# Optimization experiments

Hardware: AMD Instinct MI355X
Metric: run time of the kernel (lower is better)

Reference implementation:

```python
import jax, jax.numpy as jnp
import numpy as np

N_NODES = 50000
N_EDGES = 800000
IN_DIM = 128
HID = 32
HEADS = 3
OUT_DIM = 128
NEG_SLOPE = 0.2  # PyG GATConv default leaky_relu slope
EPS = 1e-16


def setup_inputs() -> dict:
    key = jax.random.key(0)
    ks = jax.random.split(key, 16)
    x = jax.random.normal(ks[0], (N_NODES, IN_DIM), jnp.float32)
    edge_index = jax.random.randint(ks[1], (2, N_EDGES), 0, N_NODES, dtype=jnp.int32)
    s = 0.1
    return {
        'x': x,
        'edge_index': edge_index,
        # layer 1: in=128 -> heads=3, c=32, concat
        'W1': jax.random.normal(ks[2], (IN_DIM, HEADS * HID), jnp.float32) * s,
        'as1': jax.random.normal(ks[3], (HEADS, HID), jnp.float32) * s,
        'ad1': jax.random.normal(ks[4], (HEADS, HID), jnp.float32) * s,
        'b1': jnp.zeros((HEADS * HID,), jnp.float32),
        # layer 2: in=96 -> heads=3, c=32, concat
        'W2': jax.random.normal(ks[5], (HEADS * HID, HEADS * HID), jnp.float32) * s,
        'as2': jax.random.normal(ks[6], (HEADS, HID), jnp.float32) * s,
        'ad2': jax.random.normal(ks[7], (HEADS, HID), jnp.float32) * s,
        'b2': jnp.zeros((HEADS * HID,), jnp.float32),
        # layer 3: in=96 -> heads=1, c=128, mean (concat=False)
        'W3': jax.random.normal(ks[8], (HEADS * HID, OUT_DIM), jnp.float32) * s,
        'as3': jax.random.normal(ks[9], (1, OUT_DIM), jnp.float32) * s,
        'ad3': jax.random.normal(ks[10], (1, OUT_DIM), jnp.float32) * s,
        'b3': jnp.zeros((OUT_DIM,), jnp.float32),
    }


def _gat_layer(x, src, dst, W, a_s, a_d, b, concat):
    # x: [N, F_in]; src/dst: [E'] (self-loops already appended)
    n = x.shape[0]
    heads, c = a_s.shape
    h = (x @ W).reshape(n, heads, c)                      # [N, H, C]
    alpha_src = jnp.sum(h * a_s[None], axis=-1)           # [N, H]
    alpha_dst = jnp.sum(h * a_d[None], axis=-1)           # [N, H]
    e = jax.nn.leaky_relu(alpha_src[src] + alpha_dst[dst], NEG_SLOPE)  # [E', H]
    # segment softmax over incoming edges of each dst node
    m = jax.ops.segment_max(e, dst, num_segments=n)       # [N, H] (every node has a self-loop)
    e = jnp.exp(e - m[dst])
    denom = jax.ops.segment_sum(e, dst, num_segments=n)   # [N, H]
    alpha = e / (denom[dst] + EPS)                        # [E', H]
    # attention dropout: module is evaluated in inference mode -> identity
    out = jax.ops.segment_sum(alpha[:, :, None] * h[src], dst, num_segments=n)  # [N, H, C]
    out = out.reshape(n, heads * c) if concat else out.mean(axis=1)
    return out + b


def reference(x, edge_index, W1, as1, ad1, b1, W2, as2, ad2, b2, W3, as3, ad3, b3):
    n = x.shape[0]
    loops = jnp.arange(n, dtype=edge_index.dtype)
    src = jnp.concatenate([edge_index[0], loops])  # PyG add_self_loops=True
    dst = jnp.concatenate([edge_index[1], loops])
    h = _gat_layer(x, src, dst, W1, as1, ad1, b1, concat=True)
    h = jax.nn.elu(h)
    h = _gat_layer(h, src, dst, W2, as2, ad2, b2, concat=True)
    h = jax.nn.elu(h)
    out = _gat_layer(h, src, dst, W3, as3, ad3, b3, concat=False)
    return out
```

## Files before the change

### kernel.cpp

```cpp
#include <hip/hip_runtime.h>
#include <hip/hip_bf16.h>
#include <hip/hip_fp16.h>
#include <math.h>

#define N_NODES_C 50000
#define NBKT ((N_NODES_C + 255) / 256)
#define NEG_SLOPE 0.2f
#define EPS_ 1e-16f

typedef _Float16 f16x8 __attribute__((ext_vector_type(8)));
typedef float    f32x4 __attribute__((ext_vector_type(4)));

__device__ __forceinline__ float lrelu(float x){ return x > 0.f ? x : NEG_SLOPE * x; }

__global__ void hist_k(const int* __restrict__ dstv, int* __restrict__ counts, int E){
  int t = blockIdx.x * blockDim.x + threadIdx.x;
  if (t < E) atomicAdd(&counts[dstv[t]], 1);
}

__global__ void chunksum_k(const int* __restrict__ counts, int* __restrict__ sums, int n){
  __shared__ int lds[4];
  int base = blockIdx.x * 1024;
  int t = threadIdx.x;
  int s = 0;
  for (int i = t; i < 1024; i += 256){ int idx = base + i; s += (idx < n) ? counts[idx] : 0; }
  for (int d = 32; d >= 1; d >>= 1) s += __shfl_xor(s, d);
  if ((t & 63) == 0) lds[t >> 6] = s;
  __syncthreads();
  if (t == 0) sums[blockIdx.x] = lds[0] + lds[1] + lds[2] + lds[3];
}

__global__ void scan_k(const int* __restrict__ counts, const int* __restrict__ csums,
                       int* __restrict__ row_ptr, int* __restrict__ bcur, int nch, int n){
  __shared__ int ws[16];
  __shared__ int boff;
  int base = blockIdx.x * 1024; int t = threadIdx.x; int idx = base + t;
  int v = (idx < n) ? counts[idx] : 0;
  int lane = t & 63, wid = t >> 6;
  int x = v;
  for (int d = 1; d < 64; d <<= 1){ int y = __shfl_up(x, d); if (lane >= d) x += y; }
  if (lane == 63) ws[wid] = x;
  if (t < 64){
    int c = (t < blockIdx.x) ? csums[t] : 0;
    for (int d = 32; d >= 1; d >>= 1) c += __shfl_xor(c, d);
    if (t == 0) boff = c;
  }
  __syncthreads();
  if (t < 16){ int y = ws[t]; for (int d = 1; d < 16; d <<= 1){ int z = __shfl_up(y, d); if (t >= d) y += z; } ws[t] = y; }
  __syncthreads();
  int excl = x - v + (wid ? ws[wid - 1] : 0) + boff;
  if (idx < n){
    row_ptr[idx] = excl;
    if ((idx & 255) == 0) bcur[idx >> 8] = excl;
  }
  if (blockIdx.x == nch - 1 && t == 0) row_ptr[n] = boff + ws[15];
}

#define BATCH 2048
#define BCAP 32
__global__ __launch_bounds__(256) void bucket_k(const int* __restrict__ srcv, const int* __restrict__ dstv,
                                                int* __restrict__ bcur, unsigned* __restrict__ ebuf, int E){
  __shared__ unsigned stage[NBKT * BCAP];
  __shared__ int cnt[NBKT];
  int t = threadIdx.x;
  int start = blockIdx.x * BATCH;
  int end = start + BATCH; if (end > E) end = E;
  for (int i = t; i < NBKT; i += 256) cnt[i] = 0;
  __syncthreads();
  for (int e = start + t; e < end; e += 256){
    int s = srcv[e], d = dstv[e];
    int b = d >> 8;
    unsigned entry = (unsigned)s | ((unsigned)(d & 255) << 16);
    int pos = atomicAdd(&cnt[b], 1);
    if (pos < BCAP) stage[b * BCAP + pos] = entry;
    else { int p = atomicAdd(&bcur[b], 1); ebuf[p] = entry; }
  }
  __syncthreads();
  if (t < NBKT){
    int c = cnt[t]; if (c > BCAP) c = BCAP;
    if (c > 0){
      int p = atomicAdd(&bcur[t], c);
      for (int i = 0; i < c; i++) ebuf[p + i] = stage[t * BCAP + i];
    }
  }
}

__global__ __launch_bounds__(256) void bsort_k(const unsigned* __restrict__ ebuf,
                                               const int* __restrict__ row_ptr,
                                               int* __restrict__ esrc, int n){
  __shared__ int cnt[256];
  int b = blockIdx.x;
  int nb = b * 256;
  int t = threadIdx.x;
  cnt[t] = 0;
  __syncthreads();
  int hi_node = nb + 256; if (hi_node > n) hi_node = n;
  int beg = row_ptr[nb], end = row_ptr[hi_node];
  for (int i = beg + t; i < end; i += 256){
    unsigned e = ebuf[i];
    int dl = e >> 16;
    int src = (int)(e & 0xFFFFu);
    int rank = atomicAdd(&cnt[dl], 1);
    esrc[row_ptr[nb + dl] + rank] = src;
  }
}

template<int K, int J>
__device__ void wpack_dev(const float* __restrict__ W, uint4* __restrict__ Wf, int blk, int nblk){
  constexpr int KS = K / 32, NT = J / 16;
  int tot = KS * NT * 64;
  for (int t = blk * 256 + threadIdx.x; t < tot; t += nblk * 256){
    int l = t & 63;
    int nt = (t >> 6) % NT;
    int kk = t / (64 * NT);
    int col = nt * 16 + (l & 15);
    int k0 = kk * 32 + (l >> 4) * 8;
    unsigned u[4];
    #pragma unroll
    for (int p = 0; p < 4; p++){
      __half2 h = __floats2half2_rn(W[(k0 + 2 * p) * J + col], W[(k0 + 2 * p + 1) * J + col]);
      u[p] = *reinterpret_cast<unsigned*>(&h);
    }
    uint4 v; v.x = u[0]; v.y = u[1]; v.z = u[2]; v.w = u[3];
    Wf[t] = v;
  }
}

__global__ void wpack_all_k(const float* W1, const float* W2, const float* W3,
                            uint4* Wf1, uint4* Wf2, uint4* Wf3){
  int b = blockIdx.x;
  if (b < 6) wpack_dev<128, 96>(W1, Wf1, b, 6);
  else if (b < 11) wpack_dev<96, 96>(W2, Wf2, b - 6, 5);
  else wpack_dev<96, 128>(W3, Wf3, b - 11, 6);
}

template<int K, int J, int HEADS, bool AF16>
__global__ __launch_bounds__(256) void gemm_mfma_k(
    const void* __restrict__ Ain, const uint4* __restrict__ Wf,
    const float* __restrict__ a_s, const float* __restrict__ a_d,
    __half* __restrict__ Hh, float* __restrict__ asrc, float* __restrict__ adst, int n){
  constexpr int KS = K / 32;
  constexpr int NT = J / 16;
  constexpr int CPR = K / 8;
  constexpr int NTPH = NT / HEADS;
  __shared__ uint4 Alds[64 * 16];
  int t = threadIdx.x;
  int rbase = blockIdx.x * 64;

  for (int i = t; i < 64 * CPR; i += 256){
    int r = i / CPR, c = i % CPR;
    int gr = rbase + r;
    uint4 v = make_uint4(0u, 0u, 0u, 0u);
    if (gr < n){
      if (AF16){
        v = ((const uint4*)Ain)[(size_t)gr * CPR + c];
      } else {
        const float4* af = (const float4*)Ain + (size_t)gr * (K / 4) + c * 2;
        float4 lo = af[0], hi = af[1];
        __half2 p0 = __floats2half2_rn(lo.x, lo.y);
        __half2 p1 = __floats2half2_rn(lo.z, lo.w);
        __half2 p2 = __floats2half2_rn(hi.x, hi.y);
        __half2 p3 = __floats2half2_rn(hi.z, hi.w);
        v.x = *reinterpret_cast<unsigned*>(&p0);
        v.y = *reinterpret_cast<unsigned*>(&p1);
        v.z = *reinterpret_cast<unsigned*>(&p2);
        v.w = *reinterpret_cast<unsigned*>(&p3);
      }
    }
    Alds[r * 16 + (c ^ (r & 7))] = v;
  }
  __syncthreads();

  int l = t & 63;
  int wrow = (t >> 6) * 16;
  int sub = l & 15;
  int lk = l >> 4;
  f32x4 acc[NT];
  #pragma unroll
  for (int i = 0; i < NT; i++) acc[i] = (f32x4){0.f, 0.f, 0.f, 0.f};

  for (int kk = 0; kk < KS; kk++){
    int trow = wrow + sub;
    int c = kk * 4 + lk;
    f16x8 a = *reinterpret_cast<const f16x8*>(&Alds[trow * 16 + (c ^ (trow & 7))]);
    const uint4* wb = Wf + (size_t)(kk * NT) * 64 + l;
    #pragma unroll
    for (int nt = 0; nt < NT; nt++){
      uint4 wv = wb[nt * 64];
      f16x8 bfr = *reinterpret_cast<const f16x8*>(&wv);
      acc[nt] = __builtin_amdgcn_mfma_f32_16x16x32_f16(a, bfr, acc[nt], 0, 0, 0);
    }
  }

  float ps[HEADS][4], pd[HEADS][4];
  #pragma unroll
  for (int h = 0; h < HEADS; h++)
    #pragma unroll
    for (int r = 0; r < 4; r++){ ps[h][r] = 0.f; pd[h][r] = 0.f; }
  #pragma unroll
  for (int nt = 0; nt < NT; nt++){
    int h = nt / NTPH;
    float sa = a_s[nt * 16 + sub];
    float sd = a_d[nt * 16 + sub];
    #pragma unroll
    for (int r = 0; r < 4; r++){ ps[h][r] += acc[nt][r] * sa; pd[h][r] += acc[nt][r] * sd; }
  }
  #pragma unroll
  for (int h = 0; h < HEADS; h++)
    #pragma unroll
    for (int r = 0; r < 4; r++)
      #pragma unroll
      for (int d = 1; d < 16; d <<= 1){
        ps[h][r] += __shfl_xor(ps[h][r], d);
        pd[h][r] += __shfl_xor(pd[h][r], d);
      }

  #pragma unroll
  for (int r = 0; r < 4; r++){
    int gr = rbase + wrow + lk * 4 + r;
    if (gr < n){
      #pragma unroll
      for (int nt = 0; nt < NT; nt++)
        Hh[(size_t)gr * J + nt * 16 + sub] = __float2half(acc[nt][r]);
    }
  }
  #pragma unroll
  for (int h = 0; h < HEADS; h++){
    if (sub == h){
      #pragma unroll
      for (int r = 0; r < 4; r++){
        int gr = rbase + wrow + lk * 4 + r;
        if (gr < n){
          asrc[gr * HEADS + h] = ps[h][r];
          adst[gr * HEADS + h] = pd[h][r];
        }
      }
    }
  }
}

template<int HEADS, int C, bool ELU, bool OUT16>
__global__ void agg_k(const __half* __restrict__ Hh,
                      const float* __restrict__ asrc, const float* __restrict__ adst,
                      const int* __restrict__ row_ptr, const int* __restrict__ esrc,
                      const float* __restrict__ bias, void* __restrict__ outv, int n){
  constexpr int J = HEADS * C;
  constexpr int NL = J / 2;
  constexpr int WL0 = 64 - 8 * HEADS;
  int node = blockIdx.x * (blockDim.x >> 6) + (threadIdx.x >> 6);
  if (node >= n) return;
  int lane = threadIdx.x & 63;
  bool colact = (NL == 64) || (lane < NL);
  int cl = colact ? lane : 0;
  int c0 = 2 * cl;
  int hh = c0 / C;
  const __half2* hp = (const __half2*)Hh;

  int wl = lane - WL0; if (wl < 0) wl = 0;
  int wu, wh;
  if (HEADS == 3){ wu = wl / 3; wh = wl - wu * 3; } else { wu = wl; wh = 0; }

  float ad_own = adst[node * HEADS + hh];
  float ad_w = (HEADS == 3) ? __shfl(ad_own, wh * 16) : ad_own;

  float wself = __expf(lrelu(asrc[node * HEADS + hh] + ad_own));
  float2 hs = __half22float2(hp[(size_t)node * NL + cl]);
  float acc0 = wself * hs.x, acc1 = wself * hs.y, den = wself;

  int beg = row_ptr[node], end = row_ptr[node + 1];
  int e = beg;
  for (; e + 8 <= end; e += 8){
    int s0 = esrc[e],     s1 = esrc[e + 1], s2 = esrc[e + 2], s3 = esrc[e + 3];
    int s4 = esrc[e + 4], s5 = esrc[e + 5], s6 = esrc[e + 6], s7 = esrc[e + 7];
    int ssel = wu < 4 ? (wu < 2 ? (wu == 0 ? s0 : s1) : (wu == 2 ? s2 : s3))
                      : (wu < 6 ? (wu == 4 ? s4 : s5) : (wu == 6 ? s6 : s7));
    float wv = __expf(lrelu(asrc[ssel * HEADS + wh] + ad_w));
    float w0 = __shfl(wv, WL0 + 0 * HEADS + hh);
    float w1 = __shfl(wv, WL0 + 1 * HEADS + hh);
    float w2 = __shfl(wv, WL0 + 2 * HEADS + hh);
    float w3 = __shfl(wv, WL0 + 3 * HEADS + hh);
    float w4 = __shfl(wv, WL0 + 4 * HEADS + hh);
    float w5 = __shfl(wv, WL0 + 5 * HEADS + hh);
    float w6 = __shfl(wv, WL0 + 6 * HEADS + hh);
    float w7 = __shfl(wv, WL0 + 7 * HEADS + hh);
    __half2 u0 = hp[(size_t)s0 * NL + cl];
    __half2 u1 = hp[(size_t)s1 * NL + cl];
    __half2 u2 = hp[(size_t)s2 * NL + cl];
    __half2 u3 = hp[(size_t)s3 * NL + cl];
    __half2 u4 = hp[(size_t)s4 * NL + cl];
    __half2 u5 = hp[(size_t)s5 * NL + cl];
    __half2 u6 = hp[(size_t)s6 * NL + cl];
    __half2 u7 = hp[(size_t)s7 * NL + cl];
    float2 f0 = __half22float2(u0), f1 = __half22float2(u1);
    float2 f2 = __half22float2(u2), f3 = __half22float2(u3);
    float2 f4 = __half22float2(u4), f5 = __half22float2(u5);
    float2 f6 = __half22float2(u6), f7 = __half22float2(u7);
    acc0 += w0 * f0.x; acc1 += w0 * f0.y; den += w0;
    acc0 += w1 * f1.x; acc1 += w1 * f1.y; den += w1;
    acc0 += w2 * f2.x; acc1 += w2 * f2.y; den += w2;
    acc0 += w3 * f3.x; acc1 += w3 * f3.y; den += w3;
    acc0 += w4 * f4.x; acc1 += w4 * f4.y; den += w4;
    acc0 += w5 * f5.x; acc1 += w5 * f5.y; den += w5;
    acc0 += w6 * f6.x; acc1 += w6 * f6.y; den += w6;
    acc0 += w7 * f7.x; acc1 += w7 * f7.y; den += w7;
  }
  for (; e < end; e++){
    int s = esrc[e];
    float w = __expf(lrelu(asrc[s * HEADS + hh] + ad_own));
    float2 h = __half22float2(hp[(size_t)s * NL + cl]);
    acc0 += w * h.x; acc1 += w * h.y; den += w;
  }
  if (colact){
    float inv = 1.f / (den + EPS_);
    float r0 = acc0 * inv + bias[c0];
    float r1 = acc1 * inv + bias[c0 + 1];
    if (ELU){
      r0 = r0 > 0.f ? r0 : __expf(r0) - 1.f;
      r1 = r1 > 0.f ? r1 : __expf(r1) - 1.f;
    }
    if (OUT16){
      ((__half2*)outv)[(size_t)node * NL + cl] = __floats2half2_rn(r0, r1);
    } else {
      *reinterpret_cast<float2*>((float*)outv + (size_t)node * J + c0) = make_float2(r0, r1);
    }
  }
}

extern "C" void kernel_launch(void* const* d_in, const int* in_sizes, int n_in,
                              void* d_out, int out_size, void* d_ws, size_t ws_size,
                              hipStream_t stream){
  const float* x   = (const float*)d_in[0];
  const int*   ei  = (const int*)  d_in[1];
  const float* W1  = (const float*)d_in[2];
  const float* as1 = (const float*)d_in[3];
  const float* ad1 = (const float*)d_in[4];
  const float* b1  = (const float*)d_in[5];
  const float* W2  = (const float*)d_in[6];
  const float* as2 = (const float*)d_in[7];
  const float* ad2 = (const float*)d_in[8];
  const float* b2  = (const float*)d_in[9];
  const float* W3  = (const float*)d_in[10];
  const float* as3 = (const float*)d_in[11];
  const float* ad3 = (const float*)d_in[12];
  const float* b3  = (const float*)d_in[13];
  float* out = (float*)d_out;

  const int N = N_NODES_C;
  const int E = in_sizes[1] / 2;
  const int* srcv = ei;
  const int* dstv = ei + E;

  char* ws = (char*)d_ws;
  auto alloc = [&](size_t bytes)->char*{ char* p = ws; ws += (bytes + 255) & ~(size_t)255; return p; };
  int*      counts  = (int*)     alloc((size_t)N * 4);
  int*      row_ptr = (int*)     alloc((size_t)(N + 1) * 4);
  int*      csums   = (int*)     alloc(64 * 4);
  int*      bcur    = (int*)     alloc(NBKT * 4);
  int*      esrc    = (int*)     alloc((size_t)E * 4);
  unsigned* ebuf    = (unsigned*)alloc((size_t)E * 4);
  __half*   Hh      = (__half*)  alloc((size_t)N * 128 * 2);
  __half*   feat_h  = (__half*)  alloc((size_t)N * 96 * 2);
  float*    a_src   = (float*)   alloc((size_t)N * 3 * 4);
  float*    a_dst   = (float*)   alloc((size_t)N * 3 * 4);
  uint4*    Wf1     = (uint4*)   alloc(128 * 96 * 2);
  uint4*    Wf2     = (uint4*)   alloc(96 * 96 * 2);
  uint4*    Wf3     = (uint4*)   alloc(96 * 128 * 2);

  hipMemsetAsync(counts, 0, (size_t)N * 4, stream);
  hist_k<<<(E + 255) / 256, 256, 0, stream>>>(dstv, counts, E);
  int nch = (N + 1023) / 1024;
  chunksum_k<<<nch, 256, 0, stream>>>(counts, csums, N);
  scan_k<<<nch, 1024, 0, stream>>>(counts, csums, row_ptr, bcur, nch, N);
  bucket_k<<<(E + BATCH - 1) / BATCH, 256, 0, stream>>>(srcv, dstv, bcur, ebuf, E);
  bsort_k<<<NBKT, 256, 0, stream>>>(ebuf, row_ptr, esrc, N);

  wpack_all_k<<<17, 256, 0, stream>>>(W1, W2, W3, Wf1, Wf2, Wf3);

  int gnode4 = (N + 3) / 4;
  int ggemm  = (N + 63) / 64;

  gemm_mfma_k<128, 96, 3, false><<<ggemm, 256, 0, stream>>>(x, Wf1, as1, ad1, Hh, a_src, a_dst, N);
  agg_k<3, 32, true, true><<<gnode4, 256, 0, stream>>>(Hh, a_src, a_dst, row_ptr, esrc, b1, feat_h, N);

  gemm_mfma_k<96, 96, 3, true><<<ggemm, 256, 0, stream>>>(feat_h, Wf2, as2, ad2, Hh, a_src, a_dst, N);
  agg_k<3, 32, true, true><<<gnode4, 256, 0, stream>>>(Hh, a_src, a_dst, row_ptr, esrc, b2, feat_h, N);

  gemm_mfma_k<96, 128, 1, true><<<ggemm, 256, 0, stream>>>(feat_h, Wf3, as3, ad3, Hh, a_src, a_dst, N);
  agg_k<1, 128, false, false><<<gnode4, 256, 0, stream>>>(Hh, a_src, a_dst, row_ptr, esrc, b3, out, N);
}
```

Measured before the change: 326.8 us.

## Aggregate a group of consecutive nodes per wave over a merged edge stream

Self-loops now go into the CSR itself: counts start at 1 and bucket_k emits the loop edges. Each esrc entry keeps the local destination index in its high bits, so every edge's logit is computed from asrc and adst directly. Each wavefront now handles eight consecutive nodes and walks their combined edge range with an 8-wide unrolled loop, writing out each node when its boundary is crossed. The aim is to cut idle lanes and tail loops on low-degree nodes; the cost is the cross-lane weight sharing being dropped, extra per-edge adst loads and a divergent boundary check.

```diff
diff --git a/kernel.cpp b/kernel.cpp
--- a/kernel.cpp
+++ b/kernel.cpp
@@ -12,6 +12,11 @@
 typedef float    f32x4 __attribute__((ext_vector_type(4)));
 
 __device__ __forceinline__ float lrelu(float x){ return x > 0.f ? x : NEG_SLOPE * x; }
+
+__global__ void cinit_k(int* __restrict__ counts, int n){
+  int t = blockIdx.x * blockDim.x + threadIdx.x;
+  if (t < n) counts[t] = 1;
+}
 
 __global__ void hist_k(const int* __restrict__ dstv, int* __restrict__ counts, int E){
   int t = blockIdx.x * blockDim.x + threadIdx.x;
@@ -59,16 +64,20 @@
 #define BATCH 2048
 #define BCAP 32
 __global__ __launch_bounds__(256) void bucket_k(const int* __restrict__ srcv, const int* __restrict__ dstv,
-                                                int* __restrict__ bcur, unsigned* __restrict__ ebuf, int E){
+                                                int* __restrict__ bcur, unsigned* __restrict__ ebuf,
+                                                int E, int n){
   __shared__ unsigned stage[NBKT * BCAP];
   __shared__ int cnt[NBKT];
   int t = threadIdx.x;
+  int tot = E + n;
   int start = blockIdx.x * BATCH;
-  int end = start + BATCH; if (end > E) end = E;
+  int end = start + BATCH; if (end > tot) end = tot;
   for (int i = t; i < NBKT; i += 256) cnt[i] = 0;
   __syncthreads();
-  for (int e = start + t; e < end; e += 256){
-    int s = srcv[e], d = dstv[e];
+  for (int idx = start + t; idx < end; idx += 256){
+    int s, d;
+    if (idx < E){ s = srcv[idx]; d = dstv[idx]; }
+    else { s = idx - E; d = s; }
     int b = d >> 8;
     unsigned entry = (unsigned)s | ((unsigned)(d & 255) << 16);
     int pos = atomicAdd(&cnt[b], 1);
@@ -99,9 +108,8 @@
   for (int i = beg + t; i < end; i += 256){
     unsigned e = ebuf[i];
     int dl = e >> 16;
-    int src = (int)(e & 0xFFFFu);
     int rank = atomicAdd(&cnt[dl], 1);
-    esrc[row_ptr[nb + dl] + rank] = src;
+    esrc[row_ptr[nb + dl] + rank] = (int)e;
   }
 }
 
@@ -239,91 +247,76 @@
   }
 }
 
-template<int HEADS, int C, bool ELU, bool OUT16>
-__global__ void agg_k(const __half* __restrict__ Hh,
-                      const float* __restrict__ asrc, const float* __restrict__ adst,
-                      const int* __restrict__ row_ptr, const int* __restrict__ esrc,
-                      const float* __restrict__ bias, void* __restrict__ outv, int n){
+template<int HEADS, int C, bool ELU, bool OUT16, int GN>
+__global__ __launch_bounds__(256) void agg_k(const __half* __restrict__ Hh,
+    const float* __restrict__ asrc, const float* __restrict__ adst,
+    const int* __restrict__ row_ptr, const int* __restrict__ esrc,
+    const float* __restrict__ bias, void* __restrict__ outv, int n){
   constexpr int J = HEADS * C;
   constexpr int NL = J / 2;
-  constexpr int WL0 = 64 - 8 * HEADS;
-  int node = blockIdx.x * (blockDim.x >> 6) + (threadIdx.x >> 6);
-  if (node >= n) return;
+  int wid = blockIdx.x * (blockDim.x >> 6) + (threadIdx.x >> 6);
+  int n0 = wid * GN;
+  if (n0 >= n) return;
   int lane = threadIdx.x & 63;
-  bool colact = (NL == 64) || (lane < NL);
-  int cl = colact ? lane : 0;
-  int c0 = 2 * cl;
+  if (lane >= NL) return;
+  int c0 = 2 * lane;
   int hh = c0 / C;
   const __half2* hp = (const __half2*)Hh;
-
-  int wl = lane - WL0; if (wl < 0) wl = 0;
-  int wu, wh;
-  if (HEADS == 3){ wu = wl / 3; wh = wl - wu * 3; } else { wu = wl; wh = 0; }
-
-  float ad_own = adst[node * HEADS + hh];
-  float ad_w = (HEADS == 3) ? __shfl(ad_own, wh * 16) : ad_own;
-
-  float wself = __expf(lrelu(asrc[node * HEADS + hh] + ad_own));
-  float2 hs = __half22float2(hp[(size_t)node * NL + cl]);
-  float acc0 = wself * hs.x, acc1 = wself * hs.y, den = wself;
-
-  int beg = row_ptr[node], end = row_ptr[node + 1];
-  int e = beg;
-  for (; e + 8 <= end; e += 8){
-    int s0 = esrc[e],     s1 = esrc[e + 1], s2 = esrc[e + 2], s3 = esrc[e + 3];
-    int s4 = esrc[e + 4], s5 = esrc[e + 5], s6 = esrc[e + 6], s7 = esrc[e + 7];
-    int ssel = wu < 4 ? (wu < 2 ? (wu == 0 ? s0 : s1) : (wu == 2 ? s2 : s3))
-                      : (wu < 6 ? (wu == 4 ? s4 : s5) : (wu == 6 ? s6 : s7));
-    float wv = __expf(lrelu(asrc[ssel * HEADS + wh] + ad_w));
-    float w0 = __shfl(wv, WL0 + 0 * HEADS + hh);
-    float w1 = __shfl(wv, WL0 + 1 * HEADS + hh);
-    float w2 = __shfl(wv, WL0 + 2 * HEADS + hh);
-    float w3 = __shfl(wv, WL0 + 3 * HEADS + hh);
-    float w4 = __shfl(wv, WL0 + 4 * HEADS + hh);
-    float w5 = __shfl(wv, WL0 + 5 * HEADS + hh);
-    float w6 = __shfl(wv, WL0 + 6 * HEADS + hh);
-    float w7 = __shfl(wv, WL0 + 7 * HEADS + hh);
-    __half2 u0 = hp[(size_t)s0 * NL + cl];
-    __half2 u1 = hp[(size_t)s1 * NL + cl];
-    __half2 u2 = hp[(size_t)s2 * NL + cl];
-    __half2 u3 = hp[(size_t)s3 * NL + cl];
-    __half2 u4 = hp[(size_t)s4 * NL + cl];
-    __half2 u5 = hp[(size_t)s5 * NL + cl];
-    __half2 u6 = hp[(size_t)s6 * NL + cl];
-    __half2 u7 = hp[(size_t)s7 * NL + cl];
-    float2 f0 = __half22float2(u0), f1 = __half22float2(u1);
-    float2 f2 = __half22float2(u2), f3 = __half22float2(u3);
-    float2 f4 = __half22float2(u4), f5 = __half22float2(u5);
-    float2 f6 = __half22float2(u6), f7 = __half22float2(u7);
-    acc0 += w0 * f0.x; acc1 += w0 * f0.y; den += w0;
-    acc0 += w1 * f1.x; acc1 += w1 * f1.y; den += w1;
-    acc0 += w2 * f2.x; acc1 += w2 * f2.y; den += w2;
-    acc0 += w3 * f3.x; acc1 += w3 * f3.y; den += w3;
-    acc0 += w4 * f4.x; acc1 += w4 * f4.y; den += w4;
-    acc0 += w5 * f5.x; acc1 += w5 * f5.y; den += w5;
-    acc0 += w6 * f6.x; acc1 += w6 * f6.y; den += w6;
-    acc0 += w7 * f7.x; acc1 += w7 * f7.y; den += w7;
-  }
-  for (; e < end; e++){
-    int s = esrc[e];
-    float w = __expf(lrelu(asrc[s * HEADS + hh] + ad_own));
-    float2 h = __half22float2(hp[(size_t)s * NL + cl]);
-    acc0 += w * h.x; acc1 += w * h.y; den += w;
-  }
-  if (colact){
+  int gcnt = min(GN, n - n0);
+  int rp = row_ptr[n0 + min(lane, gcnt)];
+  float b0 = bias[c0], b1 = bias[c0 + 1];
+  int bkt3 = (n0 & ~255) * HEADS;
+  int e = __shfl(rp, 0);
+  int eend = __shfl(rp, gcnt);
+  int g = 0;
+  int nb = __shfl(rp, 1);
+  float acc0 = 0.f, acc1 = 0.f, den = 0.f;
+  __half2* outh = (__half2*)outv;
+  float* outf = (float*)outv;
+
+  auto finalize = [&](int gg){
     float inv = 1.f / (den + EPS_);
-    float r0 = acc0 * inv + bias[c0];
-    float r1 = acc1 * inv + bias[c0 + 1];
+    float r0 = acc0 * inv + b0, r1 = acc1 * inv + b1;
     if (ELU){
       r0 = r0 > 0.f ? r0 : __expf(r0) - 1.f;
       r1 = r1 > 0.f ? r1 : __expf(r1) - 1.f;
     }
-    if (OUT16){
-      ((__half2*)outv)[(size_t)node * NL + cl] = __floats2half2_rn(r0, r1);
-    } else {
-      *reinterpret_cast<float2*>((float*)outv + (size_t)node * J + c0) = make_float2(r0, r1);
-    }
-  }
+    int node = n0 + gg;
+    if (OUT16) outh[(size_t)node * NL + lane] = __floats2half2_rn(r0, r1);
+    else *reinterpret_cast<float2*>(outf + (size_t)node * J + c0) = make_float2(r0, r1);
+    acc0 = 0.f; acc1 = 0.f; den = 0.f;
+  };
+
+  for (; e + 8 <= eend; e += 8){
+    int ev[8];
+    #pragma unroll
+    for (int u = 0; u < 8; u++) ev[u] = esrc[e + u];
+    float w[8]; float2 f[8];
+    #pragma unroll
+    for (int u = 0; u < 8; u++){
+      int s = ev[u] & 0xFFFF;
+      int dl = ((unsigned)ev[u]) >> 16;
+      float logit = asrc[s * HEADS + hh] + adst[bkt3 + dl * HEADS + hh];
+      w[u] = __expf(lrelu(logit));
+      f[u] = __half22float2(hp[(size_t)s * NL + lane]);
+    }
+    #pragma unroll
+    for (int u = 0; u < 8; u++){
+      while (e + u >= nb && g < gcnt - 1){ finalize(g); g++; nb = __shfl(rp, g + 1); }
+      acc0 += w[u] * f[u].x; acc1 += w[u] * f[u].y; den += w[u];
+    }
+  }
+  for (; e < eend; e++){
+    int ev = esrc[e];
+    int s = ev & 0xFFFF;
+    int dl = ((unsigned)ev) >> 16;
+    while (e >= nb && g < gcnt - 1){ finalize(g); g++; nb = __shfl(rp, g + 1); }
+    float logit = asrc[s * HEADS + hh] + adst[bkt3 + dl * HEADS + hh];
+    float wv = __expf(lrelu(logit));
+    float2 f = __half22float2(hp[(size_t)s * NL + lane]);
+    acc0 += wv * f.x; acc1 += wv * f.y; den += wv;
+  }
+  finalize(g);
 }
 
 extern "C" void kernel_launch(void* const* d_in, const int* in_sizes, int n_in,
@@ -356,8 +349,8 @@
   int*      row_ptr = (int*)     alloc((size_t)(N + 1) * 4);
   int*      csums   = (int*)     alloc(64 * 4);
   int*      bcur    = (int*)     alloc(NBKT * 4);
-  int*      esrc    = (int*)     alloc((size_t)E * 4);
-  unsigned* ebuf    = (unsigned*)alloc((size_t)E * 4);
+  int*      esrc    = (int*)     alloc((size_t)(E + N) * 4);
+  unsigned* ebuf    = (unsigned*)alloc((size_t)(E + N) * 4);
   __half*   Hh      = (__half*)  alloc((size_t)N * 128 * 2);
   __half*   feat_h  = (__half*)  alloc((size_t)N * 96 * 2);
   float*    a_src   = (float*)   alloc((size_t)N * 3 * 4);
@@ -366,25 +359,26 @@
   uint4*    Wf2     = (uint4*)   alloc(96 * 96 * 2);
   uint4*    Wf3     = (uint4*)   alloc(96 * 128 * 2);
 
-  hipMemsetAsync(counts, 0, (size_t)N * 4, stream);
+  cinit_k<<<(N + 255) / 256, 256, 0, stream>>>(counts, N);
   hist_k<<<(E + 255) / 256, 256, 0, stream>>>(dstv, counts, E);
   int nch = (N + 1023) / 1024;
   chunksum_k<<<nch, 256, 0, stream>>>(counts, csums, N);
   scan_k<<<nch, 1024, 0, stream>>>(counts, csums, row_ptr, bcur, nch, N);
-  bucket_k<<<(E + BATCH - 1) / BATCH, 256, 0, stream>>>(srcv, dstv, bcur, ebuf, E);
+  bucket_k<<<(E + N + BATCH - 1) / BATCH, 256, 0, stream>>>(srcv, dstv, bcur, ebuf, E, N);
   bsort_k<<<NBKT, 256, 0, stream>>>(ebuf, row_ptr, esrc, N);
 
   wpack_all_k<<<17, 256, 0, stream>>>(W1, W2, W3, Wf1, Wf2, Wf3);
 
-  int gnode4 = (N + 3) / 4;
-  int ggemm  = (N + 63) / 64;
+  const int GN = 8;
+  int gagg = ((N + GN - 1) / GN + 3) / 4;
+  int ggemm = (N + 63) / 64;
 
   gemm_mfma_k<128, 96, 3, false><<<ggemm, 256, 0, stream>>>(x, Wf1, as1, ad1, Hh, a_src, a_dst, N);
-  agg_k<3, 32, true, true><<<gnode4, 256, 0, stream>>>(Hh, a_src, a_dst, row_ptr, esrc, b1, feat_h, N);
+  agg_k<3, 32, true, true, GN><<<gagg, 256, 0, stream>>>(Hh, a_src, a_dst, row_ptr, esrc, b1, feat_h, N);
 
   gemm_mfma_k<96, 96, 3, true><<<ggemm, 256, 0, stream>>>(feat_h, Wf2, as2, ad2, Hh, a_src, a_dst, N);
-  agg_k<3, 32, true, true><<<gnode4, 256, 0, stream>>>(Hh, a_src, a_dst, row_ptr, esrc, b2, feat_h, N);
+  agg_k<3, 32, true, true, GN><<<gagg, 256, 0, stream>>>(Hh, a_src, a_dst, row_ptr, esrc, b2, feat_h, N);
 
   gemm_mfma_k<96, 128, 1, true><<<ggemm, 256, 0, stream>>>(feat_h, Wf3, as3, ad3, Hh, a_src, a_dst, N);
-  agg_k<1, 128, false, false><<<gnode4, 256, 0, stream>>>(Hh, a_src, a_dst, row_ptr, esrc, b3, out, N);
-}
+  agg_k<1, 128, false, false, GN><<<gagg, 256, 0, stream>>>(Hh, a_src, a_dst, row_ptr, esrc, b3, out, N);
+}
```

After: 424.2 us. +29.8%, slower.
